# Kernel tuning notes

Hardware: AMD Instinct MI355X
Metric: run time of the kernel (lower is better)

## Reference

```python
import jax, jax.numpy as jnp
import numpy as np

NUM_HEADS = 12
WINDOW = 128


def setup_inputs() -> dict:
    key = jax.random.key(0)
    k1, k2, k3, k4 = jax.random.split(key, 4)
    B, S, E = 2, 4096, 768
    x = jax.random.normal(k1, (B, S, E), dtype=jnp.float32)
    # nn.MultiheadAttention parameters
    w_in = jax.random.normal(k2, (3 * E, E), dtype=jnp.float32) * 0.02   # in_proj_weight
    b_in = jnp.zeros((3 * E,), dtype=jnp.float32)                        # in_proj_bias
    w_out = jax.random.normal(k3, (E, E), dtype=jnp.float32) * 0.02      # out_proj.weight
    b_out = jnp.zeros((E,), dtype=jnp.float32)                           # out_proj.bias
    return {"x": x, "w_in": w_in, "b_in": b_in, "w_out": w_out, "b_out": b_out}


def reference(x, w_in, b_in, w_out, b_out):
    B, S, E = x.shape
    H = NUM_HEADS
    D = E // H
    # fused qkv projection: x @ w_in.T + b_in -> [B, S, 3E]
    qkv = jnp.einsum('bse,fe->bsf', x, w_in) + b_in
    q, k, v = jnp.split(qkv, 3, axis=-1)
    q = q.reshape(B, S, H, D).transpose(0, 2, 1, 3)  # [B,H,S,D]
    k = k.reshape(B, S, H, D).transpose(0, 2, 1, 3)
    v = v.reshape(B, S, H, D).transpose(0, 2, 1, 3)
    scale = jnp.asarray(D, x.dtype) ** -0.5
    scores = jnp.einsum('bhqd,bhkd->bhqk', q * scale, k)  # [B,H,S,S]
    # Torch semantics: boolean attn_mask True == NOT allowed. The module sets
    # True inside the +-window band, so the band is masked out.
    idx = jnp.arange(S)
    band = jnp.abs(idx[:, None] - idx[None, :]) <= WINDOW  # True inside window
    scores = jnp.where(band[None, None, :, :], -jnp.inf, scores)
    attn = jax.nn.softmax(scores, axis=-1)
    out = jnp.einsum('bhqk,bhkd->bhqd', attn, v)  # [B,H,S,D]
    out = out.transpose(0, 2, 1, 3).reshape(B, S, E)
    return jnp.einsum('bse,fe->bsf', out, w_out) + b_out
```

## Files before the change

### kernel.cpp

```cpp
#include <hip/hip_runtime.h>
#include <hip/hip_bf16.h>
#include <stdint.h>

typedef __bf16 bf16_t;
typedef __bf16 bf16x8 __attribute__((ext_vector_type(8)));
typedef __bf16 bf16x4v __attribute__((ext_vector_type(4)));
typedef float f32x4 __attribute__((ext_vector_type(4)));

#define DEV __device__ __forceinline__

static constexpr int B_ = 2, S_ = 4096, E_ = 768, H_ = 12, D_ = 64;
static constexpr int WINDOW_ = 128;
static constexpr float QSCALE = 0.125f * 1.44269504088896f;

template<int C> struct IC { static constexpr int v = C; };

DEV float fexp2(float x) { return __builtin_amdgcn_exp2f(x); }

DEV void gload_lds16(const void* g, void* l) {
    __builtin_amdgcn_global_load_lds(
        (const __attribute__((address_space(1))) uint32_t*)g,
        (__attribute__((address_space(3))) uint32_t*)l, 16, 0, 0);
}

__global__ void k_cvt(const float* __restrict__ in, bf16_t* __restrict__ out, int n) {
    int i = (blockIdx.x * blockDim.x + threadIdx.x) * 4;
    if (i < n) {
        float4 v = *(const float4*)(in + i);
        bf16x4v o;
        o[0] = (bf16_t)v.x; o[1] = (bf16_t)v.y; o[2] = (bf16_t)v.z; o[3] = (bf16_t)v.w;
        *(bf16x4v*)(out + i) = o;
    }
}

template<int EPI>
__global__ void k_gemm(const bf16_t* __restrict__ A, const bf16_t* __restrict__ Bw,
                       const float* __restrict__ bias,
                       bf16_t* __restrict__ qb, bf16_t* __restrict__ kb, bf16_t* __restrict__ vtb,
                       float* __restrict__ outf,
                       int M, int N, int K, int mtiles) {
    __shared__ bf16_t As[128 * 64];
    __shared__ bf16_t Bs[128 * 64];
    int bid = blockIdx.x;
    int tm = bid % mtiles, tn = bid / mtiles;
    int m0 = tm * 128, n0 = tn * 128;
    int t = threadIdx.x;
    int lane = t & 63, wid = t >> 6;
    int l15 = lane & 15, l4 = lane >> 4;
    int wm = (wid & 1) * 64, wn = (wid >> 1) * 64;

    f32x4 acc[4][4];
#pragma unroll
    for (int i = 0; i < 4; ++i)
#pragma unroll
        for (int j = 0; j < 4; ++j) acc[i][j] = f32x4{0.f, 0.f, 0.f, 0.f};

    for (int kt = 0; kt < K; kt += 64) {
        __syncthreads();
#pragma unroll
        for (int c = 0; c < 4; ++c) {
            int idx = t + 256 * c;
            int row = idx >> 3, part = idx & 7;
            int kc = 8 * (part ^ (row & 7));
            gload_lds16(A + (long)(m0 + row) * K + kt + kc, (char*)As + idx * 16);
            gload_lds16(Bw + (long)(n0 + row) * K + kt + kc, (char*)Bs + idx * 16);
        }
        __syncthreads();
#pragma unroll
        for (int kk = 0; kk < 2; ++kk) {
            bf16x8 af[4], bfr[4];
#pragma unroll
            for (int i = 0; i < 4; ++i) {
                int row = wm + i * 16 + l15;
                int off = row * 128 + ((16 * (kk * 4 + l4)) ^ ((row & 7) << 4));
                af[i] = *(const bf16x8*)((const char*)As + off);
                int rowb = wn + i * 16 + l15;
                int offb = rowb * 128 + ((16 * (kk * 4 + l4)) ^ ((rowb & 7) << 4));
                bfr[i] = *(const bf16x8*)((const char*)Bs + offb);
            }
#pragma unroll
            for (int i = 0; i < 4; ++i)
#pragma unroll
                for (int j = 0; j < 4; ++j)
                    acc[i][j] = __builtin_amdgcn_mfma_f32_16x16x32_bf16(af[i], bfr[j], acc[i][j], 0, 0, 0);
        }
    }

#pragma unroll
    for (int i = 0; i < 4; ++i) {
#pragma unroll
        for (int j = 0; j < 4; ++j) {
            int n = n0 + wn + j * 16 + l15;
            float bv = bias[n];
            int mbase = m0 + wm + i * 16 + l4 * 4;
            if (EPI == 0) {
                int sel = n / 768, nn = n % 768;
                int h = nn >> 6, d = nn & 63;
                int b = mbase >> 12, s = mbase & 4095;
                if (sel == 2) {
                    bf16x4v pk;
#pragma unroll
                    for (int r = 0; r < 4; ++r) pk[r] = (bf16_t)(acc[i][j][r] + bv);
                    int pos = (s & ~31) | (((s >> 2) & 3) << 3) | (((s >> 4) & 1) << 2);
                    *(bf16x4v*)(vtb + ((long)(b * H_ + h) * D_ + d) * S_ + pos) = pk;
                } else {
                    long o = ((long)(b * H_ + h) * S_ + s) * D_ + d;
#pragma unroll
                    for (int r = 0; r < 4; ++r) {
                        float v = acc[i][j][r] + bv;
                        if (sel == 0) qb[o + (long)r * D_] = (bf16_t)(v * QSCALE);
                        else          kb[o + (long)r * D_] = (bf16_t)v;
                    }
                }
            } else {
#pragma unroll
                for (int r = 0; r < 4; ++r)
                    outf[(long)(mbase + r) * 768 + n] = acc[i][j][r] + bv;
            }
        }
    }
}

__global__ __launch_bounds__(256, 3)
void k_attn(const bf16_t* __restrict__ q, const bf16_t* __restrict__ k,
            const bf16_t* __restrict__ vt, bf16_t* __restrict__ ao) {
    __shared__ bf16_t Ksh[3][4096];
    __shared__ bf16_t Vsh[3][4096];
    int bid = blockIdx.x;
    bid = (bid & 7) * 96 + (bid >> 3);
    int bh = bid >> 5, qt = bid & 31;
    int q0 = qt * 128;
    int b = bh / H_, h = bh % H_;
    int t = threadIdx.x, lane = t & 63, wid = t >> 6;
    int l15 = lane & 15, l4 = lane >> 4;

    const bf16_t* qp = q + (long)bh * S_ * D_;
    const bf16_t* kp = k + (long)bh * S_ * D_;
    const bf16_t* vp = vt + (long)bh * D_ * S_;
    int wq = q0 + wid * 32;

    bf16x8 qf[2][2];
#pragma unroll
    for (int g = 0; g < 2; ++g) {
        int row = wq + g * 16 + l15;
        qf[g][0] = *(const bf16x8*)(qp + (long)row * 64 + 8 * l4);
        qf[g][1] = *(const bf16x8*)(qp + (long)row * 64 + 32 + 8 * l4);
    }

    int sw = (l15 & 7) << 4;
    int a0 = l15 * 128 + ((16 * l4) ^ sw);
    int a1 = a0 ^ 64;

    f32x4 o[2][4], osum[2];
    f32x4 mneg4[2];
#pragma unroll
    for (int g = 0; g < 2; ++g) {
        osum[g] = f32x4{0.f, 0.f, 0.f, 0.f};
        mneg4[g] = f32x4{0.f, 0.f, 0.f, 0.f};
#pragma unroll
        for (int ns = 0; ns < 4; ++ns) o[g][ns] = f32x4{0.f, 0.f, 0.f, 0.f};
    }

    bf16x8 onesB;
#pragma unroll
    for (int j = 0; j < 8; ++j) onesB[j] = (bf16_t)1.0f;

    int i2b = t + 256;
    int rowA = t >> 3, rowB = i2b >> 3;
    int part = t & 7;
    int koffA = rowA * 64 + 8 * (part ^ (rowA & 7));
    int koffB = rowB * 64 + 8 * (part ^ (rowB & 7));
    int voffA = rowA * S_ + 8 * (part ^ (rowA & 7));
    int voffB = rowB * S_ + 8 * (part ^ (rowB & 7));
    int qt2 = 2 * qt;
    int qg0 = wq + l15;
    int qg1 = qg0 + 16;

    auto NK = [&](int i) { return i < qt2 ? i : i + 2; };

    auto STAGE = [&](int kts, auto bufc) {
        constexpr int buf = decltype(bufc)::v;
        char* Kd = (char*)Ksh + buf * 8192 + t * 16;
        char* Vd = (char*)Vsh + buf * 8192 + t * 16;
        long ko = (long)kts << 12;
        int vo = kts << 6;
        gload_lds16(kp + ko + koffA, Kd);
        gload_lds16(kp + ko + koffB, Kd + 4096);
        gload_lds16(vp + vo + voffA, Vd);
        gload_lds16(vp + vo + voffB, Vd + 4096);
    };

    auto QK = [&](auto curc, f32x4 (*s)[4], f32x4 ci0, f32x4 ci1) {
        constexpr int cur = decltype(curc)::v;
        const char* KL = (const char*)Ksh + cur * 8192;
#pragma unroll
        for (int ks = 0; ks < 4; ++ks) {
            bf16x8 kf0 = *(const bf16x8*)(KL + a0 + ks * 2048);
            bf16x8 kf1 = *(const bf16x8*)(KL + a1 + ks * 2048);
            s[0][ks] = __builtin_amdgcn_mfma_f32_16x16x32_bf16(kf0, qf[0][0], ci0, 0, 0, 0);
            s[1][ks] = __builtin_amdgcn_mfma_f32_16x16x32_bf16(kf0, qf[1][0], ci1, 0, 0, 0);
            s[0][ks] = __builtin_amdgcn_mfma_f32_16x16x32_bf16(kf1, qf[0][1], s[0][ks], 0, 0, 0);
            s[1][ks] = __builtin_amdgcn_mfma_f32_16x16x32_bf16(kf1, qf[1][1], s[1][ks], 0, 0, 0);
        }
    };

    auto MASK = [&](int kt, f32x4 (*s)[4]) {
        int k0 = kt << 6;
#pragma unroll
        for (int ks = 0; ks < 4; ++ks) {
            int kb_ = k0 + ks * 16 + l4 * 4;
#pragma unroll
            for (int r = 0; r < 4; ++r) {
                int d0 = qg0 - (kb_ + r); int ad0 = d0 < 0 ? -d0 : d0;
                if (ad0 <= WINDOW_) s[0][ks][r] = -1e30f;
                int d1 = qg1 - (kb_ + r); int ad1 = d1 < 0 ? -d1 : d1;
                if (ad1 <= WINDOW_) s[1][ks][r] = -1e30f;
            }
        }
    };

    auto TAIL = [&](auto curc, f32x4 (*s)[4]) {
        constexpr int cur = decltype(curc)::v;
        bf16x8 pa[2][2];
#pragma unroll
        for (int g = 0; g < 2; ++g)
#pragma unroll
            for (int c = 0; c < 2; ++c) {
                pa[g][c][0] = (bf16_t)s[g][2*c][0];   pa[g][c][1] = (bf16_t)s[g][2*c][1];
                pa[g][c][2] = (bf16_t)s[g][2*c][2];   pa[g][c][3] = (bf16_t)s[g][2*c][3];
                pa[g][c][4] = (bf16_t)s[g][2*c+1][0]; pa[g][c][5] = (bf16_t)s[g][2*c+1][1];
                pa[g][c][6] = (bf16_t)s[g][2*c+1][2]; pa[g][c][7] = (bf16_t)s[g][2*c+1][3];
            }
#pragma unroll
        for (int g = 0; g < 2; ++g) {
            osum[g] = __builtin_amdgcn_mfma_f32_16x16x32_bf16(pa[g][0], onesB, osum[g], 0, 0, 0);
            osum[g] = __builtin_amdgcn_mfma_f32_16x16x32_bf16(pa[g][1], onesB, osum[g], 0, 0, 0);
        }
        const char* VL = (const char*)Vsh + cur * 8192;
#pragma unroll
        for (int ns = 0; ns < 4; ++ns) {
            bf16x8 vf0 = *(const bf16x8*)(VL + a0 + ns * 2048);
            bf16x8 vf1 = *(const bf16x8*)(VL + a1 + ns * 2048);
            o[0][ns] = __builtin_amdgcn_mfma_f32_16x16x32_bf16(pa[0][0], vf0, o[0][ns], 0, 0, 0);
            o[1][ns] = __builtin_amdgcn_mfma_f32_16x16x32_bf16(pa[1][0], vf0, o[1][ns], 0, 0, 0);
            o[0][ns] = __builtin_amdgcn_mfma_f32_16x16x32_bf16(pa[0][1], vf1, o[0][ns], 0, 0, 0);
            o[1][ns] = __builtin_amdgcn_mfma_f32_16x16x32_bf16(pa[1][1], vf1, o[1][ns], 0, 0, 0);
        }
    };

    auto body = [&](int idx, auto curc) {
        if (idx < 61) {
            STAGE(NK(idx + 1), IC<(decltype(curc)::v + 1) % 3>{});
            asm volatile("s_waitcnt vmcnt(4)" ::: "memory");
        } else {
            asm volatile("s_waitcnt vmcnt(0)" ::: "memory");
        }
        __builtin_amdgcn_s_barrier();
        __builtin_amdgcn_sched_barrier(0);

        int kt = NK(idx);
        int dk = kt - qt2;
        f32x4 s[2][4];
        QK(curc, s, mneg4[0], mneg4[1]);
        if (dk == -2 || dk == -1 || dk == 2 || dk == 3) MASK(kt, s);
#pragma unroll
        for (int g = 0; g < 2; ++g)
#pragma unroll
            for (int ks = 0; ks < 4; ++ks)
#pragma unroll
                for (int r = 0; r < 4; ++r)
                    s[g][ks][r] = fexp2(s[g][ks][r]);
        TAIL(curc, s);
    };

    STAGE(NK(0), IC<0>{});

    {
        STAGE(NK(1), IC<1>{});
        asm volatile("s_waitcnt vmcnt(4)" ::: "memory");
        __builtin_amdgcn_s_barrier();
        __builtin_amdgcn_sched_barrier(0);

        int kt = NK(0);
        int dk = kt - qt2;
        f32x4 s[2][4];
        QK(IC<0>{}, s, f32x4{0.f,0.f,0.f,0.f}, f32x4{0.f,0.f,0.f,0.f});
        if (dk == -2 || dk == -1 || dk == 2 || dk == 3) MASK(kt, s);
#pragma unroll
        for (int g = 0; g < 2; ++g) {
            float lm = -1e30f;
#pragma unroll
            for (int ks = 0; ks < 4; ++ks) {
                float a = fmaxf(fmaxf(s[g][ks][0], s[g][ks][1]), fmaxf(s[g][ks][2], s[g][ks][3]));
                lm = fmaxf(lm, a);
            }
            lm = fmaxf(lm, __shfl_xor(lm, 16));
            lm = fmaxf(lm, __shfl_xor(lm, 32));
            float m_ = fmaxf(lm, 0.0f);
            mneg4[g] = f32x4{-m_, -m_, -m_, -m_};
#pragma unroll
            for (int ks = 0; ks < 4; ++ks)
#pragma unroll
                for (int r = 0; r < 4; ++r)
                    s[g][ks][r] = fexp2(s[g][ks][r] - m_);
        }
        TAIL(IC<0>{}, s);
    }

    for (int i3 = 0; i3 < 20; ++i3) {
        body(3 * i3 + 1, IC<1>{});
        body(3 * i3 + 2, IC<2>{});
        body(3 * i3 + 3, IC<0>{});
    }
    body(61, IC<1>{});

#pragma unroll
    for (int g = 0; g < 2; ++g)
#pragma unroll
        for (int r = 0; r < 4; ++r) {
            float ir = 1.0f / osum[g][r];
            int srow2 = wq + g * 16 + l4 * 4 + r;
#pragma unroll
            for (int ns = 0; ns < 4; ++ns) {
                int e = h * 64 + ns * 16 + l15;
                ao[((long)b * S_ + srow2) * E_ + e] = (bf16_t)(o[g][ns][r] * ir);
            }
        }
}

extern "C" void kernel_launch(void* const* d_in, const int* in_sizes, int n_in,
                              void* d_out, int out_size, void* d_ws, size_t ws_size,
                              hipStream_t stream) {
    const float* x     = (const float*)d_in[0];
    const float* w_in  = (const float*)d_in[1];
    const float* b_in  = (const float*)d_in[2];
    const float* w_out = (const float*)d_in[3];
    const float* b_out = (const float*)d_in[4];
    float* out = (float*)d_out;

    char* ws = (char*)d_ws;
    bf16_t* xb  = (bf16_t*)(ws + 0);
    bf16_t* wib = (bf16_t*)(ws + 12582912);
    bf16_t* wob = (bf16_t*)(ws + 16121856);
    bf16_t* qb  = (bf16_t*)(ws + 17301504);
    bf16_t* kb  = (bf16_t*)(ws + 29884416);
    bf16_t* vtb = (bf16_t*)(ws + 42467328);
    bf16_t* ao  = xb;

    k_cvt<<<6144, 256, 0, stream>>>(x, xb, 6291456);
    k_cvt<<<1728, 256, 0, stream>>>(w_in, wib, 1769472);
    k_cvt<<<576, 256, 0, stream>>>(w_out, wob, 589824);

    k_gemm<0><<<64 * 18, 256, 0, stream>>>(xb, wib, b_in, qb, kb, vtb, nullptr,
                                           8192, 2304, 768, 64);
    k_attn<<<24 * 32, 256, 0, stream>>>(qb, kb, vtb, ao);
    k_gemm<1><<<64 * 6, 256, 0, stream>>>(ao, wob, b_out, nullptr, nullptr, nullptr, out,
                                          8192, 768, 768, 64);
}
```

Measured before the change: 184.5 us.

## Split attention key range across two blocks and merge partials in combine kernel

Each query tile's 62 key tiles are split into two halves processed by separate blocks, doubling the grid from 768 to 1536 blocks. Each block writes unnormalized bf16 partial outputs plus row sums and running max, and a new combine kernel rescales and merges them into the attention output. LDS buffering drops from triple to double, with an extra barrier after each iteration, so occupancy can rise to 5 blocks per CU. The aim is better CU utilisation on the 256-CU part. The cost is an extra launch, extra partial-output memory traffic, and bf16 rounding of the unnormalized partials.

```diff
diff --git a/kernel.cpp b/kernel.cpp
--- a/kernel.cpp
+++ b/kernel.cpp
@@ -121,22 +121,27 @@
     }
 }
 
-__global__ __launch_bounds__(256, 3)
-void k_attn(const bf16_t* __restrict__ q, const bf16_t* __restrict__ k,
-            const bf16_t* __restrict__ vt, bf16_t* __restrict__ ao) {
-    __shared__ bf16_t Ksh[3][4096];
-    __shared__ bf16_t Vsh[3][4096];
-    int bid = blockIdx.x;
-    bid = (bid & 7) * 96 + (bid >> 3);
-    int bh = bid >> 5, qt = bid & 31;
+__global__ __launch_bounds__(256, 5)
+void k_attn_part(const bf16_t* __restrict__ q, const bf16_t* __restrict__ k,
+                 const bf16_t* __restrict__ vt,
+                 bf16_t* __restrict__ p0, bf16_t* __restrict__ p1,
+                 float* __restrict__ sums) {
+    __shared__ bf16_t Ksh[2][4096];
+    __shared__ bf16_t Vsh[2][4096];
+    int raw = blockIdx.x;
+    int sw_ = (raw & 7) * 192 + (raw >> 3);
+    int strm = sw_ & 1;
+    int id = sw_ >> 1;
+    int bh = id >> 5, qt = id & 31;
     int q0 = qt * 128;
-    int b = bh / H_, h = bh % H_;
     int t = threadIdx.x, lane = t & 63, wid = t >> 6;
     int l15 = lane & 15, l4 = lane >> 4;
 
     const bf16_t* qp = q + (long)bh * S_ * D_;
     const bf16_t* kp = k + (long)bh * S_ * D_;
     const bf16_t* vp = vt + (long)bh * D_ * S_;
+    bf16_t* po = strm ? p1 : p0;
+    int soff = strm * (24 * S_) + bh * S_;
     int wq = q0 + wid * 32;
 
     bf16x8 qf[2][2];
@@ -175,6 +180,7 @@
     int qt2 = 2 * qt;
     int qg0 = wq + l15;
     int qg1 = qg0 + 16;
+    int tbase = strm * 31;
 
     auto NK = [&](int i) { return i < qt2 ? i : i + 2; };
 
@@ -248,9 +254,9 @@
         }
     };
 
-    auto body = [&](int idx, auto curc) {
-        if (idx < 61) {
-            STAGE(NK(idx + 1), IC<(decltype(curc)::v + 1) % 3>{});
+    auto body = [&](int off, auto curc) {
+        if (off < 30) {
+            STAGE(NK(tbase + off + 1), IC<(decltype(curc)::v) ^ 1>{});
             asm volatile("s_waitcnt vmcnt(4)" ::: "memory");
         } else {
             asm volatile("s_waitcnt vmcnt(0)" ::: "memory");
@@ -258,7 +264,7 @@
         __builtin_amdgcn_s_barrier();
         __builtin_amdgcn_sched_barrier(0);
 
-        int kt = NK(idx);
+        int kt = NK(tbase + off);
         int dk = kt - qt2;
         f32x4 s[2][4];
         QK(curc, s, mneg4[0], mneg4[1]);
@@ -271,17 +277,19 @@
                 for (int r = 0; r < 4; ++r)
                     s[g][ks][r] = fexp2(s[g][ks][r]);
         TAIL(curc, s);
+        __builtin_amdgcn_sched_barrier(0);
+        __builtin_amdgcn_s_barrier();
     };
 
-    STAGE(NK(0), IC<0>{});
+    STAGE(NK(tbase), IC<0>{});
 
     {
-        STAGE(NK(1), IC<1>{});
+        STAGE(NK(tbase + 1), IC<1>{});
         asm volatile("s_waitcnt vmcnt(4)" ::: "memory");
         __builtin_amdgcn_s_barrier();
         __builtin_amdgcn_sched_barrier(0);
 
-        int kt = NK(0);
+        int kt = NK(tbase);
         int dk = kt - qt2;
         f32x4 s[2][4];
         QK(IC<0>{}, s, f32x4{0.f,0.f,0.f,0.f}, f32x4{0.f,0.f,0.f,0.f});
@@ -305,27 +313,61 @@
                     s[g][ks][r] = fexp2(s[g][ks][r] - m_);
         }
         TAIL(IC<0>{}, s);
-    }
-
-    for (int i3 = 0; i3 < 20; ++i3) {
-        body(3 * i3 + 1, IC<1>{});
-        body(3 * i3 + 2, IC<2>{});
-        body(3 * i3 + 3, IC<0>{});
-    }
-    body(61, IC<1>{});
+        __builtin_amdgcn_sched_barrier(0);
+        __builtin_amdgcn_s_barrier();
+    }
+
+    for (int j = 0; j < 15; ++j) {
+        body(2 * j + 1, IC<1>{});
+        body(2 * j + 2, IC<0>{});
+    }
 
 #pragma unroll
     for (int g = 0; g < 2; ++g)
 #pragma unroll
         for (int r = 0; r < 4; ++r) {
-            float ir = 1.0f / osum[g][r];
-            int srow2 = wq + g * 16 + l4 * 4 + r;
-#pragma unroll
-            for (int ns = 0; ns < 4; ++ns) {
-                int e = h * 64 + ns * 16 + l15;
-                ao[((long)b * S_ + srow2) * E_ + e] = (bf16_t)(o[g][ns][r] * ir);
-            }
-        }
+            int row = wq + g * 16 + l4 * 4 + r;
+#pragma unroll
+            for (int ns = 0; ns < 4; ++ns)
+                po[((long)bh * S_ + row) * 64 + ns * 16 + l15] = (bf16_t)(o[g][ns][r]);
+        }
+    if (l15 == 0) {
+#pragma unroll
+        for (int g = 0; g < 2; ++g)
+#pragma unroll
+            for (int r = 0; r < 4; ++r)
+                sums[soff + wq + g * 16 + l4 * 4 + r] = osum[g][r];
+    }
+    if (lane < 16) {
+#pragma unroll
+        for (int g = 0; g < 2; ++g)
+            sums[2 * 24 * S_ + soff + wq + g * 16 + l15] = -mneg4[g][0];
+    }
+}
+
+__global__ void k_combine(const bf16_t* __restrict__ p0, const bf16_t* __restrict__ p1,
+                          const float* __restrict__ sums, bf16_t* __restrict__ ao) {
+    int idx = blockIdx.x * 256 + threadIdx.x;
+    int bh = idx >> 12, s = idx & 4095;
+    int b = bh / H_, h = bh % H_;
+    const float* ms = sums + 2 * 24 * S_;
+    float m0 = ms[idx], m1 = ms[24 * S_ + idx];
+    float s0 = sums[idx], s1 = sums[24 * S_ + idx];
+    float M = fmaxf(m0, m1);
+    float f0 = fexp2(m0 - M), f1 = fexp2(m1 - M);
+    float inv = 1.0f / (s0 * f0 + s1 * f1);
+    float ca = f0 * inv, cb = f1 * inv;
+    const bf16x8* qa = (const bf16x8*)(p0 + (long)idx * 64);
+    const bf16x8* qb_ = (const bf16x8*)(p1 + (long)idx * 64);
+    bf16_t* dst = ao + ((long)b * S_ + s) * E_ + h * 64;
+#pragma unroll
+    for (int c8 = 0; c8 < 8; ++c8) {
+        bf16x8 va = qa[c8], vb = qb_[c8], r;
+#pragma unroll
+        for (int j = 0; j < 8; ++j)
+            r[j] = (bf16_t)((float)va[j] * ca + (float)vb[j] * cb);
+        *(bf16x8*)(dst + 8 * c8) = r;
+    }
 }
 
 extern "C" void kernel_launch(void* const* d_in, const int* in_sizes, int n_in,
@@ -345,7 +387,10 @@
     bf16_t* qb  = (bf16_t*)(ws + 17301504);
     bf16_t* kb  = (bf16_t*)(ws + 29884416);
     bf16_t* vtb = (bf16_t*)(ws + 42467328);
-    bf16_t* ao  = xb;
+    bf16_t* p0  = (bf16_t*)(ws + 55050240);
+    bf16_t* p1  = xb;
+    float*  sums = (float*)wib;
+    bf16_t* ao  = qb;
 
     k_cvt<<<6144, 256, 0, stream>>>(x, xb, 6291456);
     k_cvt<<<1728, 256, 0, stream>>>(w_in, wib, 1769472);
@@ -353,7 +398,8 @@
 
     k_gemm<0><<<64 * 18, 256, 0, stream>>>(xb, wib, b_in, qb, kb, vtb, nullptr,
                                            8192, 2304, 768, 64);
-    k_attn<<<24 * 32, 256, 0, stream>>>(qb, kb, vtb, ao);
+    k_attn_part<<<24 * 32 * 2, 256, 0, stream>>>(qb, kb, vtb, p0, p1, sums);
+    k_combine<<<384, 256, 0, stream>>>(p0, p1, sums, ao);
     k_gemm<1><<<64 * 6, 256, 0, stream>>>(ao, wob, b_out, nullptr, nullptr, nullptr, out,
                                           8192, 768, 768, 64);
 }
```

Result: slower. 422.3 us (+128.9%).
